# Performance work log

Measured on AMD Instinct MI355X. Metric: run time of the kernel, lower is better.

## Reference

```python
import jax, jax.numpy as jnp
import numpy as np

NUM_EMBS = 1024
EMB_DIM = 128
Z_SHAPE = (16, 4096, EMB_DIM)


def setup_inputs() -> dict:
    key = jax.random.key(0)
    k_z, k_c = jax.random.split(key)
    z = jax.random.normal(k_z, Z_SHAPE, dtype=jnp.float32)
    # torch init: uniform(-1/num_embs, 1/num_embs)
    codebook = jax.random.uniform(
        k_c, (NUM_EMBS, EMB_DIM), dtype=jnp.float32,
        minval=-1.0 / NUM_EMBS, maxval=1.0 / NUM_EMBS)
    return {"z": z, "codebook": codebook}


def reference(z, codebook):
    """Vector quantization forward (nbooks=1, balance=False).

    Returns (z_q with straight-through estimator, quant_loss, commit_loss, indices).
    """
    K, D = codebook.shape
    zf = z.reshape(-1, D)  # [M, D]
    dist = (
        jnp.sum(zf * zf, axis=1, keepdims=True)
        - 2.0 * (zf @ codebook.T)
        + jnp.sum(codebook * codebook, axis=1)[None, :]
    )
    idx = jnp.argmin(dist, axis=1)  # [M]
    # one-hot @ codebook == gather (same math, efficient form)
    z_q = codebook[idx].reshape(z.shape)
    quant_loss = jnp.mean((jax.lax.stop_gradient(z_q) - z) ** 2, axis=-1)
    commit_loss = jnp.mean((z_q - jax.lax.stop_gradient(z)) ** 2, axis=-1)
    # straight-through estimator
    z_q_ste = z + jax.lax.stop_gradient(z_q - z)
    indices = idx.reshape(z.shape[:-1])
    return z_q_ste, quant_loss, commit_loss, indices
```

## Files before the change

kernel.cpp:

```cpp
#include <hip/hip_runtime.h>
#include <hip/hip_bf16.h>

namespace {
constexpr int D       = 128;
constexpr int K       = 1024;
constexpr int M_TOTAL = 65536;
constexpr int BM      = 128;
constexpr int NCT     = K / 16;
constexpr float TAU   = 5.0e-5f;
constexpr size_t WS_CN   = 0;
constexpr size_t WS_BH   = 4096;
constexpr size_t WS_BL   = 4096 + 262144;
constexpr size_t WS_REQ  = 4096 + 2 * 262144;
constexpr size_t WS_CBT  = WS_REQ;
constexpr size_t WS_REQ2 = WS_REQ + 524288;
}

typedef short bf16x8 __attribute__((ext_vector_type(8)));
typedef float f32x4  __attribute__((ext_vector_type(4)));

static __device__ __forceinline__ unsigned short bfbits(float x) {
  __hip_bfloat16 h = __float2bfloat16(x);
  return *reinterpret_cast<unsigned short*>(&h);
}
static __device__ __forceinline__ float bfhi2f(unsigned short h) {
  return __uint_as_float(((unsigned)h) << 16);
}
static __device__ __forceinline__ void split8(float4 a, float4 b,
                                              bf16x8& ph, bf16x8& pl) {
  float v[8] = {a.x, a.y, a.z, a.w, b.x, b.y, b.z, b.w};
#pragma unroll
  for (int e = 0; e < 8; ++e) {
    unsigned short h = bfbits(v[e]);
    unsigned short l = bfbits(v[e] - bfhi2f(h));
    ph[e] = (short)h;
    pl[e] = (short)l;
  }
}
static __device__ __forceinline__ float np_norm128(const float* p) {
  float r8[8];
#pragma unroll
  for (int j = 0; j < 8; ++j) r8[j] = __fmul_rn(p[j], p[j]);
  for (int i = 8; i < D; i += 8) {
#pragma unroll
    for (int j = 0; j < 8; ++j)
      r8[j] = __fadd_rn(r8[j], __fmul_rn(p[i + j], p[i + j]));
  }
  return __fadd_rn(__fadd_rn(__fadd_rn(r8[0], r8[1]), __fadd_rn(r8[2], r8[3])),
                   __fadd_rn(__fadd_rn(r8[4], r8[5]), __fadd_rn(r8[6], r8[7])));
}

__global__ void vq_prep_all(const float* __restrict__ cb, float* __restrict__ Cn,
                            int* __restrict__ cnt,
                            short* __restrict__ Bh, short* __restrict__ Bl,
                            float4* __restrict__ cbT4) {
  const int b = blockIdx.x, t = threadIdx.x;
  if (b < 4) {
    int k = b * 256 + t;
    if (b == 0 && t == 0) *cnt = 0;
    if (k < K) Cn[k] = np_norm128(cb + (size_t)k * D);
  } else if (b < 68) {
    int g = (b - 4) * 256 + t;
    int code = (g >> 8) * 16 + (g & 15);
    int d0   = ((g >> 6) & 3) * 32 + ((g >> 4) & 3) * 8;
    const float* p = cb + (size_t)code * D + d0;
    float4 a = *reinterpret_cast<const float4*>(p);
    float4 bb = *reinterpret_cast<const float4*>(p + 4);
    bf16x8 ph, pl;
    split8(a, bb, ph, pl);
    *reinterpret_cast<bf16x8*>(Bh + (size_t)g * 8) = ph;
    *reinterpret_cast<bf16x8*>(Bl + (size_t)g * 8) = pl;
  } else {
    int g = (b - 68) * 256 + t;
    int d = g >> 8, tt = g & 255;
    float4 v;
    v.x = cb[(size_t)(4 * tt + 0) * D + d];
    v.y = cb[(size_t)(4 * tt + 1) * D + d];
    v.z = cb[(size_t)(4 * tt + 2) * D + d];
    v.w = cb[(size_t)(4 * tt + 3) * D + d];
    cbT4[g] = v;
  }
}

__global__ __launch_bounds__(256, 2) void vq_score(
    const float* __restrict__ z, const float* __restrict__ Cn,
    const short* __restrict__ BhG, const short* __restrict__ BlG,
    float* __restrict__ out_iF, int* __restrict__ cnt, int* __restrict__ list) {
  __shared__ __align__(16) short Bbuf[4][2][8][512];
  __shared__ float CnS[K];

  const int t    = threadIdx.x;
  const int wave = t >> 6;
  const int lane = t & 63;
  const int col  = lane & 15;
  const int baseRow = blockIdx.x * BM;

  for (int i = t; i < K; i += 256) CnS[i] = Cn[i];

  bf16x8 ah[2][4], al[2][4];
#pragma unroll
  for (int set = 0; set < 2; ++set) {
    const float* zL = z + (size_t)(baseRow + wave * 32 + set * 16 + col) * D + (lane >> 4) * 8;
#pragma unroll
    for (int ks = 0; ks < 4; ++ks) {
      float4 a = *reinterpret_cast<const float4*>(zL + ks * 32);
      float4 b = *reinterpret_cast<const float4*>(zL + ks * 32 + 4);
      split8(a, b, ah[set][ks], al[set][ks]);
    }
  }

  float s1[2][4], s2[2][4]; int i1[2][4];
#pragma unroll
  for (int s = 0; s < 2; ++s)
#pragma unroll
    for (int i = 0; i < 4; ++i) {
      s1[s][i] = 3.402823466e+38f; s2[s][i] = 3.402823466e+38f; i1[s][i] = 0;
    }

#define STAGE(ct_, db_)                                                             \
  { _Pragma("unroll")                                                               \
    for (int c_ = 0; c_ < 8; ++c_) {                                                \
      int p_  = c_ >> 2, ks_ = c_ & 3;                                              \
      const short* gsrc_ = (p_ ? BlG : BhG) +                                       \
                           (size_t)(((ct_) * 4 + ks_) * 64 + lane) * 8;             \
      __builtin_amdgcn_global_load_lds(                                             \
          (const __attribute__((address_space(1))) void*)gsrc_,                     \
          (__attribute__((address_space(3))) void*)&Bbuf[wave][db_][c_][0], 16, 0, 0); \
    } }

#define COMP(db_, ct_)                                                              \
  { bf16x8 bh_c[4], bl_c[4];                                                        \
    _Pragma("unroll")                                                               \
    for (int ks_ = 0; ks_ < 4; ++ks_) {                                             \
      bh_c[ks_] = *reinterpret_cast<const bf16x8*>(&Bbuf[wave][db_][ks_][lane * 8]);     \
      bl_c[ks_] = *reinterpret_cast<const bf16x8*>(&Bbuf[wave][db_][4 + ks_][lane * 8]); \
    }                                                                               \
    const int code_ = (ct_) * 16 + col;                                             \
    const float cn_ = CnS[code_];                                                   \
    __builtin_amdgcn_s_setprio(1);                                                  \
    _Pragma("unroll")                                                               \
    for (int set_ = 0; set_ < 2; ++set_) {                                          \
      f32x4 aA = (f32x4){0.f,0.f,0.f,0.f};                                          \
      f32x4 aB = (f32x4){0.f,0.f,0.f,0.f};                                          \
      f32x4 aC = (f32x4){0.f,0.f,0.f,0.f};                                          \
      _Pragma("unroll")                                                             \
      for (int ks_ = 0; ks_ < 4; ++ks_) {                                           \
        aA = __builtin_amdgcn_mfma_f32_16x16x32_bf16(ah[set_][ks_], bh_c[ks_], aA, 0,0,0); \
        aB = __builtin_amdgcn_mfma_f32_16x16x32_bf16(ah[set_][ks_], bl_c[ks_], aB, 0,0,0); \
        aC = __builtin_amdgcn_mfma_f32_16x16x32_bf16(al[set_][ks_], bh_c[ks_], aC, 0,0,0); \
      }                                                                             \
      _Pragma("unroll")                                                             \
      for (int reg_ = 0; reg_ < 4; ++reg_) {                                        \
        float S = fmaf(-2.0f, (aA[reg_] + aB[reg_]) + aC[reg_], cn_);               \
        if (S < s1[set_][reg_]) { s2[set_][reg_] = s1[set_][reg_];                  \
                                  s1[set_][reg_] = S; i1[set_][reg_] = code_; }     \
        else if (S < s2[set_][reg_]) { s2[set_][reg_] = S; }                        \
      }                                                                             \
    }                                                                               \
    __builtin_amdgcn_s_setprio(0); }

#define WAIT8  { asm volatile("s_waitcnt vmcnt(8)" ::: "memory"); \
                 __builtin_amdgcn_sched_barrier(0); }
#define WAIT0  { asm volatile("s_waitcnt vmcnt(0)" ::: "memory"); \
                 __builtin_amdgcn_sched_barrier(0); }

  __syncthreads();
  STAGE(0, 0); STAGE(1, 1);
  for (int g = 0; g < NCT - 2; g += 2) {
    WAIT8;  COMP(0, g);      STAGE(g + 2, 0);
    WAIT8;  COMP(1, g + 1);  STAGE(g + 3, 1);
  }
  WAIT8;  COMP(0, NCT - 2);
  WAIT0;  COMP(1, NCT - 1);
#undef WAIT8
#undef WAIT0
#undef STAGE
#undef COMP

#pragma unroll
  for (int m = 1; m < 16; m <<= 1) {
#pragma unroll
    for (int set = 0; set < 2; ++set)
#pragma unroll
      for (int reg = 0; reg < 4; ++reg) {
        float os1 = __shfl_xor(s1[set][reg], m, 64);
        float os2 = __shfl_xor(s2[set][reg], m, 64);
        int   oi  = __shfl_xor(i1[set][reg], m, 64);
        if (os1 < s1[set][reg]) {
          s2[set][reg] = fminf(s1[set][reg], os2);
          s1[set][reg] = os1; i1[set][reg] = oi;
        } else {
          s2[set][reg] = fminf(s2[set][reg], os1);
        }
      }
  }

  if (col == 0) {
#pragma unroll
    for (int set = 0; set < 2; ++set)
#pragma unroll
      for (int reg = 0; reg < 4; ++reg) {
        int row = wave * 32 + set * 16 + (lane >> 4) * 4 + reg;
        size_t m = (size_t)baseRow + row;
        out_iF[m] = (float)i1[set][reg];
        if (s2[set][reg] - s1[set][reg] < TAU) {
          int p = atomicAdd(cnt, 1);
          if (p < M_TOTAL - 1) list[p] = (int)m;
        }
      }
  }
}

__global__ __launch_bounds__(256, 4) void vq_rescan_cbT(
    const float* __restrict__ z, const float4* __restrict__ cbT4,
    const float* __restrict__ Cn,
    const int* __restrict__ cnt, const int* __restrict__ list,
    float* __restrict__ out_iF) {
  __shared__ __align__(16) float Zs[D];
  __shared__ float sRed[256];
  __shared__ int   iRed[256];
  const int t = threadIdx.x;
  int n = *cnt; if (n > M_TOTAL - 1) n = M_TOTAL - 1;

  for (int it = blockIdx.x; it < n; it += gridDim.x) {
    const int row = list[it];
    if (t < 32) {
      reinterpret_cast<float4*>(Zs)[t] =
          reinterpret_cast<const float4*>(z + (size_t)row * D)[t];
    }
    __syncthreads();

    float a0 = 0.f, a1 = 0.f, a2 = 0.f, a3 = 0.f;
#pragma unroll 8
    for (int d = 0; d < D; ++d) {
      float  zv = Zs[d];
      float4 cv = cbT4[(d << 8) + t];
      a0 = fmaf(zv, cv.x, a0);
      a1 = fmaf(zv, cv.y, a1);
      a2 = fmaf(zv, cv.z, a2);
      a3 = fmaf(zv, cv.w, a3);
    }
    const float A = np_norm128(Zs);

    const int kb = t * 4;
    float bd = 3.402823466e+38f; int bi = 0;
    {
      float d0 = __fadd_rn(__fsub_rn(A, __fmul_rn(2.0f, a0)), Cn[kb + 0]);
      float d1 = __fadd_rn(__fsub_rn(A, __fmul_rn(2.0f, a1)), Cn[kb + 1]);
      float d2 = __fadd_rn(__fsub_rn(A, __fmul_rn(2.0f, a2)), Cn[kb + 2]);
      float d3 = __fadd_rn(__fsub_rn(A, __fmul_rn(2.0f, a3)), Cn[kb + 3]);
      if (d0 < bd) { bd = d0; bi = kb + 0; }
      if (d1 < bd) { bd = d1; bi = kb + 1; }
      if (d2 < bd) { bd = d2; bi = kb + 2; }
      if (d3 < bd) { bd = d3; bi = kb + 3; }
    }
    sRed[t] = bd; iRed[t] = bi;
    __syncthreads();
    for (int w = 128; w > 0; w >>= 1) {
      if (t < w) {
        float o = sRed[t + w]; int oi = iRed[t + w];
        if (o < sRed[t] || (o == sRed[t] && oi < iRed[t])) { sRed[t] = o; iRed[t] = oi; }
      }
      __syncthreads();
    }
    if (t == 0) out_iF[row] = (float)iRed[0];
    __syncthreads();
  }
}

__global__ __launch_bounds__(256) void vq_epi(
    const float* __restrict__ z, const float* __restrict__ cb,
    const float* __restrict__ out_iF,
    float* __restrict__ out_zq, float* __restrict__ out_q,
    float* __restrict__ out_c) {
  const int t = threadIdx.x;
  const int r = t >> 2, q = t & 3;
  const size_t m = (size_t)blockIdx.x * 64 + r;
  const int idx = (int)out_iF[m];
  const float4* cq = reinterpret_cast<const float4*>(cb + (size_t)idx * D);
  const float4* zr = reinterpret_cast<const float4*>(z + m * D);
  float4*       o4 = reinterpret_cast<float4*>(out_zq + m * D);
  float sum = 0.f;
#pragma unroll
  for (int e = 0; e < 8; ++e) {
    int d4 = q * 8 + e;
    float4 cv = cq[d4];
    float4 zv = zr[d4];
    float dx = cv.x - zv.x, dy = cv.y - zv.y, dz = cv.z - zv.z, dw = cv.w - zv.w;
    float4 st;
    st.x = zv.x + dx; st.y = zv.y + dy; st.z = zv.z + dz; st.w = zv.w + dw;
    o4[d4] = st;
    sum = fmaf(dx, dx, sum); sum = fmaf(dy, dy, sum);
    sum = fmaf(dz, dz, sum); sum = fmaf(dw, dw, sum);
  }
  sum += __shfl_xor(sum, 1, 64);
  sum += __shfl_xor(sum, 2, 64);
  if (q == 0) {
    float lv = sum * 0.0078125f;
    out_q[m] = lv;
    out_c[m] = lv;
  }
}

__global__ __launch_bounds__(256) void vq_main_fp32(
    const float* __restrict__ z, const float* __restrict__ cb,
    const float* __restrict__ Cn,
    float* __restrict__ out_zq, float* __restrict__ out_q,
    float* __restrict__ out_c, float* __restrict__ out_i) {
  __shared__ float Zt[64 * D];
  __shared__ float Ct[64 * D];
  __shared__ float Arow[64];
  __shared__ int   idxArr[64];

  const int t  = threadIdx.x;
  const int ty = t >> 4;
  const int tx = t & 15;
  const int baseRow = blockIdx.x * 64;

  for (int s = t; s < 64 * (D / 4); s += 256) {
    int r = s >> 5, d4 = s & 31;
    float4 v = reinterpret_cast<const float4*>(z)[(size_t)(baseRow + r) * (D / 4) + d4];
    int colx = d4 ^ (r & 7);
    *reinterpret_cast<float4*>(&Zt[r * D + colx * 4]) = v;
  }
  __syncthreads();

  if (t < 64) {
    const int rs = t & 7;
    float r8[8];
#pragma unroll
    for (int j = 0; j < 8; ++j) {
      float v = Zt[t * D + (((j >> 2) ^ rs) << 2) + (j & 3)];
      r8[j] = __fmul_rn(v, v);
    }
    for (int i = 8; i < D; i += 8) {
#pragma unroll
      for (int j = 0; j < 8; ++j) {
        int d = i + j;
        float v = Zt[t * D + (((d >> 2) ^ rs) << 2) + (d & 3)];
        r8[j] = __fadd_rn(r8[j], __fmul_rn(v, v));
      }
    }
    Arow[t] = __fadd_rn(__fadd_rn(__fadd_rn(r8[0], r8[1]), __fadd_rn(r8[2], r8[3])),
                        __fadd_rn(__fadd_rn(r8[4], r8[5]), __fadd_rn(r8[6], r8[7])));
  }

  float s1[4]; int i1[4];
#pragma unroll
  for (int i = 0; i < 4; ++i) { s1[i] = 3.402823466e+38f; i1[i] = 0; }

  const int zsw = ty & 7;
  const int csw = tx & 7;

  for (int kt = 0; kt < 16; ++kt) {
    __syncthreads();
    for (int s = t; s < 64 * (D / 4); s += 256) {
      int r = s >> 5, d4 = s & 31;
      float4 v = reinterpret_cast<const float4*>(cb)[(size_t)(kt * 64 + r) * (D / 4) + d4];
      int colx = d4 ^ (r & 7);
      *reinterpret_cast<float4*>(&Ct[r * D + colx * 4]) = v;
    }
    __syncthreads();

    float acc[4][4];
#pragma unroll
    for (int i = 0; i < 4; ++i)
#pragma unroll
      for (int j = 0; j < 4; ++j) acc[i][j] = 0.f;

    for (int d4 = 0; d4 < 32; ++d4) {
      float4 za[4], cv[4];
      int zc = (d4 ^ zsw) * 4;
      int cc = (d4 ^ csw) * 4;
#pragma unroll
      for (int i = 0; i < 4; ++i)
        za[i] = *reinterpret_cast<const float4*>(&Zt[(ty + 16 * i) * D + zc]);
#pragma unroll
      for (int j = 0; j < 4; ++j)
        cv[j] = *reinterpret_cast<const float4*>(&Ct[(tx + 16 * j) * D + cc]);
#pragma unroll
      for (int i = 0; i < 4; ++i)
#pragma unroll
        for (int j = 0; j < 4; ++j) {
          acc[i][j] = fmaf(za[i].x, cv[j].x, acc[i][j]);
          acc[i][j] = fmaf(za[i].y, cv[j].y, acc[i][j]);
          acc[i][j] = fmaf(za[i].z, cv[j].z, acc[i][j]);
          acc[i][j] = fmaf(za[i].w, cv[j].w, acc[i][j]);
        }
    }

    float ch[4]; int kg[4];
#pragma unroll
    for (int j = 0; j < 4; ++j) {
      kg[j] = kt * 64 + tx + 16 * j;
      ch[j] = Cn[kg[j]];
    }
#pragma unroll
    for (int i = 0; i < 4; ++i) {
      float a = Arow[ty + 16 * i];
#pragma unroll
      for (int j = 0; j < 4; ++j) {
        float dist = __fadd_rn(__fsub_rn(a, __fmul_rn(2.0f, acc[i][j])), ch[j]);
        if (dist < s1[i]) { s1[i] = dist; i1[i] = kg[j]; }
      }
    }
  }

#pragma unroll
  for (int m = 1; m < 16; m <<= 1) {
#pragma unroll
    for (int i = 0; i < 4; ++i) {
      float os = __shfl_xor(s1[i], m, 64);
      int   oi = __shfl_xor(i1[i], m, 64);
      if (os < s1[i] || (os == s1[i] && oi < i1[i])) { s1[i] = os; i1[i] = oi; }
    }
  }

  if (tx == 0) {
#pragma unroll
    for (int i = 0; i < 4; ++i) idxArr[ty + 16 * i] = i1[i];
  }
  __syncthreads();

  {
    int r = t >> 2, q = t & 3;
    int idx = idxArr[r];
    size_t m = (size_t)baseRow + r;
    const float4* cq = reinterpret_cast<const float4*>(cb + (size_t)idx * D);
    const float4* zr = reinterpret_cast<const float4*>(z + m * D);
    float4*       o4 = reinterpret_cast<float4*>(out_zq + m * D);
    float sum = 0.f;
#pragma unroll
    for (int e = 0; e < 8; ++e) {
      int d4 = q * 8 + e;
      float4 cv = cq[d4];
      float4 zv = zr[d4];
      float dx = cv.x - zv.x, dy = cv.y - zv.y, dz = cv.z - zv.z, dw = cv.w - zv.w;
      float4 st;
      st.x = zv.x + dx; st.y = zv.y + dy; st.z = zv.z + dz; st.w = zv.w + dw;
      o4[d4] = st;
      sum = fmaf(dx, dx, sum); sum = fmaf(dy, dy, sum);
      sum = fmaf(dz, dz, sum); sum = fmaf(dw, dw, sum);
    }
    sum += __shfl_xor(sum, 1, 64);
    sum += __shfl_xor(sum, 2, 64);
    if (q == 0) {
      float lv = sum * 0.0078125f;
      out_q[m] = lv;
      out_c[m] = lv;
      out_i[m] = (float)idx;
    }
  }
}

extern "C" void kernel_launch(void* const* d_in, const int* in_sizes, int n_in,
                              void* d_out, int out_size, void* d_ws, size_t ws_size,
                              hipStream_t stream) {
  const float* z  = (const float*)d_in[0];
  const float* cb = (const float*)d_in[1];

  float* out0 = (float*)d_out;
  float* out1 = out0 + (size_t)M_TOTAL * D;
  float* out2 = out1 + M_TOTAL;
  float* out3 = out2 + M_TOTAL;

  float* Cn = (float*)((char*)d_ws + WS_CN);
  int* cnt  = (int*)out2;
  int* list = (int*)out2 + 1;

  if (ws_size >= WS_REQ2) {
    short*  Bh   = (short*)((char*)d_ws + WS_BH);
    short*  Bl   = (short*)((char*)d_ws + WS_BL);
    float4* cbT4 = (float4*)((char*)d_ws + WS_CBT);
    vq_prep_all<<<196, 256, 0, stream>>>(cb, Cn, cnt, Bh, Bl, cbT4);
    vq_score<<<M_TOTAL / BM, 256, 0, stream>>>(z, Cn, Bh, Bl, out3, cnt, list);
    vq_rescan_cbT<<<1024, 256, 0, stream>>>(z, cbT4, Cn, cnt, list, out3);
    vq_epi<<<M_TOTAL / 64, 256, 0, stream>>>(z, cb, out3, out0, out1, out2);
  } else {
    vq_prep_all<<<4, 256, 0, stream>>>(cb, Cn, cnt, nullptr, nullptr, nullptr);
    vq_main_fp32<<<M_TOTAL / 64, 256, 0, stream>>>(z, cb, Cn, out0, out1, out2, out3);
  }
}
```

Baseline: 120.2 us.

## Halve LDS staging buffers with half-tile pipeline and raise occupancy to four blocks

Splits each 16-code tile's B staging into two K-halves, so the per-wave double buffer holds 4 chunks instead of 8. This halves the LDS footprint of the score kernel, and launch bounds are raised to 4 blocks per CU to hide latency with more waves. The accumulators now live across the two half-steps and argmin tracking happens after both halves. The risks are register pressure from the higher occupancy target, which may cause spills, and the finer-grained waits reducing overlap within a wave.

```diff
diff --git a/kernel.cpp b/kernel.cpp
--- a/kernel.cpp
+++ b/kernel.cpp
@@ -82,11 +82,11 @@
   }
 }
 
-__global__ __launch_bounds__(256, 2) void vq_score(
+__global__ __launch_bounds__(256, 4) void vq_score(
     const float* __restrict__ z, const float* __restrict__ Cn,
     const short* __restrict__ BhG, const short* __restrict__ BlG,
     float* __restrict__ out_iF, int* __restrict__ cnt, int* __restrict__ list) {
-  __shared__ __align__(16) short Bbuf[4][2][8][512];
+  __shared__ __align__(16) short Bbuf[4][2][4][512];
   __shared__ float CnS[K];
 
   const int t    = threadIdx.x;
@@ -117,65 +117,80 @@
       s1[s][i] = 3.402823466e+38f; s2[s][i] = 3.402823466e+38f; i1[s][i] = 0;
     }
 
-#define STAGE(ct_, db_)                                                             \
+#define STAGE_H(ct_, h_, db_)                                                       \
   { _Pragma("unroll")                                                               \
-    for (int c_ = 0; c_ < 8; ++c_) {                                                \
-      int p_  = c_ >> 2, ks_ = c_ & 3;                                              \
+    for (int cc_ = 0; cc_ < 4; ++cc_) {                                             \
+      int p_  = cc_ >> 1, ks_ = 2 * (h_) + (cc_ & 1);                               \
       const short* gsrc_ = (p_ ? BlG : BhG) +                                       \
                            (size_t)(((ct_) * 4 + ks_) * 64 + lane) * 8;             \
       __builtin_amdgcn_global_load_lds(                                             \
           (const __attribute__((address_space(1))) void*)gsrc_,                     \
-          (__attribute__((address_space(3))) void*)&Bbuf[wave][db_][c_][0], 16, 0, 0); \
+          (__attribute__((address_space(3))) void*)&Bbuf[wave][db_][cc_][0], 16, 0, 0); \
     } }
 
-#define COMP(db_, ct_)                                                              \
-  { bf16x8 bh_c[4], bl_c[4];                                                        \
+#define COMP_H(db_, h_)                                                             \
+  { __builtin_amdgcn_s_setprio(1);                                                  \
     _Pragma("unroll")                                                               \
-    for (int ks_ = 0; ks_ < 4; ++ks_) {                                             \
-      bh_c[ks_] = *reinterpret_cast<const bf16x8*>(&Bbuf[wave][db_][ks_][lane * 8]);     \
-      bl_c[ks_] = *reinterpret_cast<const bf16x8*>(&Bbuf[wave][db_][4 + ks_][lane * 8]); \
+    for (int j_ = 0; j_ < 2; ++j_) {                                                \
+      int ks_ = 2 * (h_) + j_;                                                      \
+      bf16x8 bh_c = *reinterpret_cast<const bf16x8*>(&Bbuf[wave][db_][j_][lane * 8]);     \
+      bf16x8 bl_c = *reinterpret_cast<const bf16x8*>(&Bbuf[wave][db_][2 + j_][lane * 8]); \
+      _Pragma("unroll")                                                             \
+      for (int set_ = 0; set_ < 2; ++set_) {                                        \
+        aA[set_] = __builtin_amdgcn_mfma_f32_16x16x32_bf16(ah[set_][ks_], bh_c, aA[set_], 0,0,0); \
+        aB[set_] = __builtin_amdgcn_mfma_f32_16x16x32_bf16(ah[set_][ks_], bl_c, aB[set_], 0,0,0); \
+        aC[set_] = __builtin_amdgcn_mfma_f32_16x16x32_bf16(al[set_][ks_], bh_c, aC[set_], 0,0,0); \
+      }                                                                             \
     }                                                                               \
-    const int code_ = (ct_) * 16 + col;                                             \
+    __builtin_amdgcn_s_setprio(0); }
+
+#define TRACK(ct_)                                                                  \
+  { const int code_ = (ct_) * 16 + col;                                             \
     const float cn_ = CnS[code_];                                                   \
-    __builtin_amdgcn_s_setprio(1);                                                  \
     _Pragma("unroll")                                                               \
     for (int set_ = 0; set_ < 2; ++set_) {                                          \
-      f32x4 aA = (f32x4){0.f,0.f,0.f,0.f};                                          \
-      f32x4 aB = (f32x4){0.f,0.f,0.f,0.f};                                          \
-      f32x4 aC = (f32x4){0.f,0.f,0.f,0.f};                                          \
-      _Pragma("unroll")                                                             \
-      for (int ks_ = 0; ks_ < 4; ++ks_) {                                           \
-        aA = __builtin_amdgcn_mfma_f32_16x16x32_bf16(ah[set_][ks_], bh_c[ks_], aA, 0,0,0); \
-        aB = __builtin_amdgcn_mfma_f32_16x16x32_bf16(ah[set_][ks_], bl_c[ks_], aB, 0,0,0); \
-        aC = __builtin_amdgcn_mfma_f32_16x16x32_bf16(al[set_][ks_], bh_c[ks_], aC, 0,0,0); \
-      }                                                                             \
       _Pragma("unroll")                                                             \
       for (int reg_ = 0; reg_ < 4; ++reg_) {                                        \
-        float S = fmaf(-2.0f, (aA[reg_] + aB[reg_]) + aC[reg_], cn_);               \
+        float S = fmaf(-2.0f, (aA[set_][reg_] + aB[set_][reg_]) + aC[set_][reg_], cn_); \
         if (S < s1[set_][reg_]) { s2[set_][reg_] = s1[set_][reg_];                  \
                                   s1[set_][reg_] = S; i1[set_][reg_] = code_; }     \
         else if (S < s2[set_][reg_]) { s2[set_][reg_] = S; }                        \
       }                                                                             \
-    }                                                                               \
-    __builtin_amdgcn_s_setprio(0); }
-
-#define WAIT8  { asm volatile("s_waitcnt vmcnt(8)" ::: "memory"); \
+    } }
+
+#define ZERO_ACC                                                                    \
+  { _Pragma("unroll")                                                               \
+    for (int s_ = 0; s_ < 2; ++s_) {                                                \
+      aA[s_] = (f32x4){0.f,0.f,0.f,0.f};                                            \
+      aB[s_] = (f32x4){0.f,0.f,0.f,0.f};                                            \
+      aC[s_] = (f32x4){0.f,0.f,0.f,0.f};                                            \
+    } }
+
+#define WAIT4  { asm volatile("s_waitcnt vmcnt(4)" ::: "memory"); \
                  __builtin_amdgcn_sched_barrier(0); }
 #define WAIT0  { asm volatile("s_waitcnt vmcnt(0)" ::: "memory"); \
                  __builtin_amdgcn_sched_barrier(0); }
 
+  f32x4 aA[2], aB[2], aC[2];
+
   __syncthreads();
-  STAGE(0, 0); STAGE(1, 1);
-  for (int g = 0; g < NCT - 2; g += 2) {
-    WAIT8;  COMP(0, g);      STAGE(g + 2, 0);
-    WAIT8;  COMP(1, g + 1);  STAGE(g + 3, 1);
-  }
-  WAIT8;  COMP(0, NCT - 2);
-  WAIT0;  COMP(1, NCT - 1);
-#undef WAIT8
+  STAGE_H(0, 0, 0); STAGE_H(0, 1, 1);
+  for (int ct = 0; ct < NCT - 1; ++ct) {
+    ZERO_ACC;
+    WAIT4;  COMP_H(0, 0);  STAGE_H(ct + 1, 0, 0);
+    WAIT4;  COMP_H(1, 1);  STAGE_H(ct + 1, 1, 1);
+    TRACK(ct);
+  }
+  ZERO_ACC;
+  WAIT4;  COMP_H(0, 0);
+  WAIT0;  COMP_H(1, 1);
+  TRACK(NCT - 1);
+#undef WAIT4
 #undef WAIT0
-#undef STAGE
-#undef COMP
+#undef STAGE_H
+#undef COMP_H
+#undef TRACK
+#undef ZERO_ACC
 
 #pragma unroll
   for (int m = 1; m < 16; m <<= 1) {
```

After: 171.3 us. 42.4% more time.
